# Kernel tuning notes

Hardware: AMD Instinct MI355X
Metric: run time of the kernel (lower is better)

## Reference

```python
import jax, jax.numpy as jnp
import numpy as np

N_NODES = 50000
N_EDGES = 800000
IN_DIM = 100

def setup_inputs() -> dict:
    key = jax.random.key(0)
    ks = jax.random.split(key, 12)
    nf = jax.random.normal(ks[0], (3, IN_DIM), dtype=jnp.float32)
    tid = jax.random.randint(ks[1], (N_NODES,), 0, 4)
    xr = jax.random.normal(ks[2], (N_NODES, IN_DIM), dtype=jnp.float32)
    # nodes of type 0/1/2 get exact prototype rows; type 3 ('edge') gets random rows
    x = jnp.where((tid < 3)[:, None], nf[jnp.clip(tid, 0, 2)], xr)
    edge_index = jax.random.randint(ks[3], (2, N_EDGES), 0, N_NODES, dtype=jnp.int32)
    def w(k, fi, fo):
        return jax.random.normal(k, (fi, fo), dtype=jnp.float32) * (1.0 / np.sqrt(fi))
    return {
        'x': x, 'node_feature': nf, 'edge_index': edge_index,
        'W1': w(ks[4], 100, 512), 'b1': jnp.zeros((512,), jnp.float32),
        'W2': w(ks[5], 512, 256), 'b2': jnp.zeros((256,), jnp.float32),
        'W3': w(ks[6], 256, 128), 'b3': jnp.zeros((128,), jnp.float32),
        'W4': w(ks[7], 128, 200), 'b4': jnp.zeros((200,), jnp.float32),
    }

def _gcn_forward(x, edge_index, W1, b1, W2, b2, W3, b3, W4, b4):
    N = x.shape[0]
    loop = jnp.arange(N, dtype=edge_index.dtype)
    src = jnp.concatenate([edge_index[0], loop])
    dst = jnp.concatenate([edge_index[1], loop])
    deg = jax.ops.segment_sum(jnp.ones_like(src, dtype=x.dtype), dst, num_segments=N)
    dinv = jnp.where(deg > 0, jax.lax.rsqrt(deg), 0.0)
    norm = dinv[src] * dinv[dst]  # symmetric GCN normalization with self-loops
    def gcn(h, W, b):
        h = h @ W
        agg = jax.ops.segment_sum(h[src] * norm[:, None], dst, num_segments=N)
        return agg + b
    out = jax.nn.relu(gcn(x, W1, b1))
    out = jax.nn.relu(gcn(out, W2, b2))
    out = jax.nn.relu(gcn(out, W3, b3))
    out = jax.nn.relu(gcn(out, W4, b4))
    return out

def _cat_mean(x, out, node_feature):
    # Vectorized replacement of the per-node python loop: output slot order is
    # init(nf0)->0, accept(nf2)->1, edge(other)->2, common(nf1)->3, matching the
    # original append order when all groups are nonempty.
    eq = jnp.all(x[:, None, :] == node_feature[None, :, :], axis=-1)  # [N,3]
    group = jnp.where(eq[:, 0], 0, jnp.where(eq[:, 1], 3, jnp.where(eq[:, 2], 1, 2)))
    sums = jax.ops.segment_sum(out, group, num_segments=4)            # [4,D]
    cnt = jax.ops.segment_sum(jnp.ones((x.shape[0],), out.dtype), group, num_segments=4)
    means = jnp.where(cnt[:, None] > 0, sums / jnp.maximum(cnt, 1.0)[:, None], 0.0)
    return means.reshape(1, -1)  # [1, 4*D]

def reference(x, node_feature, edge_index, W1, b1, W2, b2, W3, b3, W4, b4):
    out = _gcn_forward(x, edge_index, W1, b1, W2, b2, W3, b3, W4, b4)
    return _cat_mean(x, out, node_feature)
```

## Files before the change

kernel.cpp:

```cpp
#include <hip/hip_runtime.h>
#include <stdint.h>

typedef __attribute__((ext_vector_type(8))) short bf16x8;
typedef __attribute__((ext_vector_type(4))) float f32x4;

__device__ __forceinline__ float bf2f(ushort h) {
    union { uint u; float f; } v; v.u = ((uint)h) << 16; return v.f;
}
__device__ __forceinline__ ushort f2bf(float f) {
    union { float f; uint u; } v; v.f = f;
    uint u = v.u;
    return (ushort)((u + 0x7fffu + ((u >> 16) & 1u)) >> 16);
}

__device__ __forceinline__ void gll(const ushort* g, ushort* l) {
    __builtin_amdgcn_global_load_lds(
        (const __attribute__((address_space(1))) void*)g,
        (__attribute__((address_space(3))) void*)l, 16, 0, 0);
}

template <int VEC>
__device__ __forceinline__ void ldbf(const ushort* p, float* v) {
    if constexpr (VEC == 4) {
        uint2 u = *(const uint2*)p;
        v[0] = bf2f((ushort)(u.x & 0xffffu));
        v[1] = bf2f((ushort)(u.x >> 16));
        v[2] = bf2f((ushort)(u.y & 0xffffu));
        v[3] = bf2f((ushort)(u.y >> 16));
    } else {
        uint4 u = *(const uint4*)p;
        v[0] = bf2f((ushort)(u.x & 0xffffu));
        v[1] = bf2f((ushort)(u.x >> 16));
        v[2] = bf2f((ushort)(u.y & 0xffffu));
        v[3] = bf2f((ushort)(u.y >> 16));
        v[4] = bf2f((ushort)(u.z & 0xffffu));
        v[5] = bf2f((ushort)(u.z >> 16));
        v[6] = bf2f((ushort)(u.w & 0xffffu));
        v[7] = bf2f((ushort)(u.w >> 16));
    }
}


__device__ __forceinline__ void tr2_one(const float* __restrict__ W,
                                        ushort* __restrict__ WTh, ushort* __restrict__ WTl,
                                        int K, int Nc, int KP, int idx) {
    int n = idx / KP, k = idx % KP;
    float w = (n < Nc && k < K) ? W[(size_t)k * Nc + n] : 0.0f;
    ushort hi = f2bf(w);
    ushort lo = f2bf(w - bf2f(hi));
    WTh[idx] = hi;
    WTl[idx] = lo;
}

__global__ void k_init(const uint* __restrict__ xu, const uint* __restrict__ nfu,
                       ushort* __restrict__ xb, int* __restrict__ gid, int NN,
                       const int* __restrict__ dst, int E, int* __restrict__ deg,
                       const float* __restrict__ W1, const float* __restrict__ W2,
                       const float* __restrict__ W3, const float* __restrict__ W4,
                       ushort* __restrict__ WT1h, ushort* __restrict__ WT1l,
                       ushort* __restrict__ WT2h, ushort* __restrict__ WT2l,
                       ushort* __restrict__ WT3h, ushort* __restrict__ WT3l,
                       ushort* __restrict__ WT4h, ushort* __restrict__ WT4l,
                       int PB, int EB) {
    int b = blockIdx.x;
    if (b < PB) {
        int wid = b * 4 + (threadIdx.x >> 6);
        int lane = threadIdx.x & 63;
        if (wid >= NN) return;
        int c0 = lane * 2;
        uint w = 0u;
        int m0 = 1, m1 = 1, m2 = 1;
        if (c0 < 100) {
            uint2 xv = *(const uint2*)&xu[(size_t)wid * 100 + c0];
            uint2 a = *(const uint2*)&nfu[c0];
            uint2 bb = *(const uint2*)&nfu[100 + c0];
            uint2 c = *(const uint2*)&nfu[200 + c0];
            m0 = (xv.x == a.x) & (xv.y == a.y);
            m1 = (xv.x == bb.x) & (xv.y == bb.y);
            m2 = (xv.x == c.x) & (xv.y == c.y);
            w = (uint)f2bf(__uint_as_float(xv.x)) | ((uint)f2bf(__uint_as_float(xv.y)) << 16);
        }
        int e0 = __all(m0), e1 = __all(m1), e2 = __all(m2);
        *(uint*)&xb[(size_t)wid * 128 + c0] = w;
        if (lane == 0) gid[wid] = e0 ? 0 : (e1 ? 3 : (e2 ? 1 : 2));
    } else if (b < PB + EB) {
        int e = (b - PB) * 256 + threadIdx.x;
        if (e < E) atomicAdd(&deg[dst[e]], 1);
    } else {
        int idx = (b - PB - EB) * 256 + threadIdx.x;
        if (idx < 65536) tr2_one(W1, WT1h, WT1l, 100, 512, 128, idx);
        else if (idx < 196608) tr2_one(W2, WT2h, WT2l, 512, 256, 512, idx - 65536);
        else if (idx < 229376) tr2_one(W3, WT3h, WT3l, 256, 128, 256, idx - 196608);
        else if (idx < 262144) tr2_one(W4, WT4h, WT4l, 128, 200, 128, idx - 229376);
    }
}


__global__ void k_scanA(const int* __restrict__ deg, int* __restrict__ offs,
                        int* __restrict__ bsum, float* __restrict__ dinv,
                        const int* __restrict__ gid, int* __restrict__ gcnt, int NN) {
    __shared__ int lds[256];
    __shared__ int cnt4[4];
    int t = threadIdx.x;
    if (t < 4) cnt4[t] = 0;
    int i = blockIdx.x * 256 + t;
    int v = (i < NN) ? deg[i] : 0;
    if (i < NN) dinv[i] = 1.0f / sqrtf((float)(v + 1));
    lds[t] = v;
    __syncthreads();
    if (i < NN) atomicAdd(&cnt4[gid[i]], 1);
    for (int d = 1; d < 256; d <<= 1) {
        int u = (t >= d) ? lds[t - d] : 0;
        __syncthreads();
        lds[t] += u;
        __syncthreads();
    }
    if (i < NN) offs[i] = lds[t] - v;
    if (t == 255) bsum[blockIdx.x] = lds[255];
    __syncthreads();
    if (t < 4 && cnt4[t]) atomicAdd(&gcnt[t], cnt4[t]);
}


__global__ void k_fill(const int* __restrict__ src, const int* __restrict__ dst, int E,
                       const float* __restrict__ dinv, const int* __restrict__ offs,
                       const int* __restrict__ bsum,
                       int* __restrict__ cur, uint2* __restrict__ epk, int NN, int NB,
                       int* __restrict__ goffs) {
    __shared__ int sex[256];
    int t = threadIdx.x;
    int v = (t < NB) ? bsum[t] : 0;
    sex[t] = v;
    __syncthreads();
    for (int d = 1; d < 256; d <<= 1) {
        int u = (t >= d) ? sex[t - d] : 0;
        __syncthreads();
        sex[t] += u;
        __syncthreads();
    }
    int incl = sex[t];
    __syncthreads();
    sex[t] = incl - v;
    __syncthreads();
    int i = blockIdx.x * 256 + t;
    if (i < NN) goffs[i] = offs[i] + sex[i >> 8];
    if (i >= E) return;
    int s = src[i], d = dst[i];
    int p = offs[d] + sex[d >> 8] + atomicAdd(&cur[d], 1);
    epk[p] = make_uint2((uint)s, __float_as_uint(dinv[s] * dinv[d]));
}


template <int D, bool BR>
__global__ void k_aggs(const ushort* __restrict__ H, ushort* __restrict__ outb,
                       const float* __restrict__ dinv, const int* __restrict__ offs,
                       const int* __restrict__ deg, const uint2* __restrict__ epk,
                       const float* __restrict__ bias, int NN, int NNpad) {
    constexpr int VEC = D / 32;
    int wid = (int)((blockIdx.x * blockDim.x + threadIdx.x) >> 6);
    int lane = threadIdx.x & 63;
    int half = lane >> 5, sl = lane & 31;
    if (wid >= NNpad) return;
    int c0 = sl * VEC;
    ushort* op = outb + (size_t)wid * D + c0;
    if (wid >= NN) {
        if (half == 0) {
            if (VEC == 4) *(uint2*)op = make_uint2(0u, 0u);
            else { uint4 z; z.x = z.y = z.z = z.w = 0u; *(uint4*)op = z; }
        }
        return;
    }
    float acc[VEC];
#pragma unroll
    for (int j = 0; j < VEC; ++j) acc[j] = 0.0f;
    int beg = offs[wid], d = deg[wid];
    if (half == 0) {
        float t0[VEC];
        ldbf<VEC>(H + (size_t)wid * D + c0, t0);
        float di = dinv[wid];
        float sw = di * di;
#pragma unroll
        for (int j = 0; j < VEC; ++j) acc[j] = sw * t0[j];
    }
    int d0 = (d + 1) >> 1;
    int e = beg + half * d0;
    int end = e + (half ? (d - d0) : d0);
    for (; e + 3 < end; e += 4) {
        uint2 q0 = epk[e], q1 = epk[e + 1], q2 = epk[e + 2], q3 = epk[e + 3];
        float t0[VEC], t1[VEC], t2[VEC], t3[VEC];
        ldbf<VEC>(H + (size_t)q0.x * D + c0, t0);
        ldbf<VEC>(H + (size_t)q1.x * D + c0, t1);
        ldbf<VEC>(H + (size_t)q2.x * D + c0, t2);
        ldbf<VEC>(H + (size_t)q3.x * D + c0, t3);
        float w0 = __uint_as_float(q0.y), w1 = __uint_as_float(q1.y);
        float w2 = __uint_as_float(q2.y), w3 = __uint_as_float(q3.y);
#pragma unroll
        for (int j = 0; j < VEC; ++j) acc[j] += w0 * t0[j];
#pragma unroll
        for (int j = 0; j < VEC; ++j) acc[j] += w1 * t1[j];
#pragma unroll
        for (int j = 0; j < VEC; ++j) acc[j] += w2 * t2[j];
#pragma unroll
        for (int j = 0; j < VEC; ++j) acc[j] += w3 * t3[j];
    }
    for (; e < end; ++e) {
        uint2 q0 = epk[e];
        float t0[VEC];
        ldbf<VEC>(H + (size_t)q0.x * D + c0, t0);
        float w0 = __uint_as_float(q0.y);
#pragma unroll
        for (int j = 0; j < VEC; ++j) acc[j] += w0 * t0[j];
    }
#pragma unroll
    for (int j = 0; j < VEC; ++j) acc[j] += __shfl_xor(acc[j], 32);
    if (half == 0) {
        ushort r[VEC];
#pragma unroll
        for (int j = 0; j < VEC; ++j) {
            float v = acc[j];
            if (BR) v = fmaxf(v + bias[c0 + j], 0.0f);
            r[j] = f2bf(v);
        }
        if (VEC == 4) {
            uint2 w;
            w.x = (uint)r[0] | ((uint)r[1] << 16);
            w.y = (uint)r[2] | ((uint)r[3] << 16);
            *(uint2*)op = w;
        } else {
            uint4 w;
            w.x = (uint)r[0] | ((uint)r[1] << 16);
            w.y = (uint)r[2] | ((uint)r[3] << 16);
            w.z = (uint)r[4] | ((uint)r[5] << 16);
            w.w = (uint)r[6] | ((uint)r[7] << 16);
            *(uint4*)op = w;
        }
    }
}


template <bool BR, int OUT>
__global__ __launch_bounds__(256) void k_gemm(
        const ushort* __restrict__ A,
        const ushort* __restrict__ Bh, const ushort* __restrict__ Bl,
        const float* __restrict__ bias,
        ushort* __restrict__ Cb,
        int Nc, int K, int tNb,
        const int* __restrict__ gid, float* __restrict__ gsum, int NN) {
    __shared__ union {
        ushort st[3][128 * 32];
        float epi[64 * 132];
    } sm;
    __shared__ int gcode[64];
    int bm = blockIdx.x / tNb, bn = blockIdx.x % tNb;
    int m0 = bm * 128, n0 = bn * 128;
    int wv = threadIdx.x >> 6, lane = threadIdx.x & 63;
    int l15 = lane & 15, quad = lane >> 4;
    const ushort* gsrc;
    ushort* ldst;
    int ng;
    if (wv == 0)      { gsrc = A  + (size_t)m0 * K;        ldst = sm.st[0];        ng = 4; }
    else if (wv == 1) { gsrc = A  + (size_t)(m0 + 64) * K; ldst = sm.st[0] + 2048; ng = 4; }
    else if (wv == 2) { gsrc = Bh + (size_t)n0 * K;        ldst = sm.st[1];        ng = 8; }
    else              { gsrc = Bl + (size_t)n0 * K;        ldst = sm.st[2];        ng = 8; }
    const ushort* gBase = gsrc + (size_t)(lane >> 2) * K + (lane & 3) * 8;
    int wm = (wv >> 1) * 64, wn = (wv & 1) * 64;
    const ushort* sA_ = sm.st[0];
    const ushort* sBh_ = sm.st[1];
    const ushort* sBl_ = sm.st[2];
    f32x4 acc[4][4] = {};
    for (int k0 = 0; k0 < K; k0 += 32) {
        for (int i = 0; i < ng; ++i)
            gll(gBase + (size_t)(16 * i) * K + k0, ldst + i * 512);
        __syncthreads();
        bf16x8 Af[4], Bfh[4], Bfl[4];
#pragma unroll
        for (int i = 0; i < 4; ++i) {
            int ra = (wm + 16 * i + l15) * 32 + quad * 8;
            int rb = (wn + 16 * i + l15) * 32 + quad * 8;
            Af[i]  = *(const bf16x8*)(sA_ + ra);
            Bfh[i] = *(const bf16x8*)(sBh_ + rb);
            Bfl[i] = *(const bf16x8*)(sBl_ + rb);
        }
#pragma unroll
        for (int mi = 0; mi < 4; ++mi)
#pragma unroll
            for (int ni = 0; ni < 4; ++ni) {
                acc[mi][ni] = __builtin_amdgcn_mfma_f32_16x16x32_bf16(Af[mi], Bfh[ni], acc[mi][ni], 0, 0, 0);
                acc[mi][ni] = __builtin_amdgcn_mfma_f32_16x16x32_bf16(Af[mi], Bfl[ni], acc[mi][ni], 0, 0, 0);
            }
        __syncthreads();
    }
    float bia[4] = {0.f, 0.f, 0.f, 0.f};
    if (BR) {
#pragma unroll
        for (int ni = 0; ni < 4; ++ni) {
            int col = n0 + wn + 16 * ni + l15;
            if (col < Nc) bia[ni] = bias[col];
        }
    }
    float* epi = sm.epi;
    int t = threadIdx.x;
    float s0 = 0.f, s1 = 0.f, s2 = 0.f, s3 = 0.f;
    int colR = t & 127, rg = t >> 7;
    for (int half = 0; half < 2; ++half) {
        if ((wv >> 1) == half) {
#pragma unroll
            for (int mi = 0; mi < 4; ++mi)
#pragma unroll
                for (int r = 0; r < 4; ++r) {
                    int rl = mi * 16 + quad * 4 + r;
#pragma unroll
                    for (int ni = 0; ni < 4; ++ni) {
                        float v = acc[mi][ni][r];
                        if (BR) v = fmaxf(v + bia[ni], 0.0f);
                        epi[rl * 132 + wn + ni * 16 + l15] = v;
                    }
                }
        }
        if (OUT == 2 && t < 64) {
            int grow = m0 + half * 64 + t;
            gcode[t] = (grow < NN) ? gid[grow] : -1;
        }
        __syncthreads();
        if (OUT == 2) {
#pragma unroll 4
            for (int r = 0; r < 32; ++r) {
                int row = rg * 32 + r;
                int g = gcode[row];
                float v = epi[row * 132 + colR];
                s0 += (g == 0) ? v : 0.f;
                s1 += (g == 1) ? v : 0.f;
                s2 += (g == 2) ? v : 0.f;
                s3 += (g == 3) ? v : 0.f;
            }
        } else {
#pragma unroll
            for (int j = 0; j < 16; ++j) {
                int e = (j * 256 + t) * 2;
                int rl = e >> 7, cl = e & 127;
                int grow = m0 + half * 64 + rl;
                int gcol = n0 + cl;
                float v0 = epi[rl * 132 + cl];
                float v1 = epi[rl * 132 + cl + 1];
                *(uint*)&Cb[(size_t)grow * Nc + gcol] = (uint)f2bf(v0) | ((uint)f2bf(v1) << 16);
            }
        }
        __syncthreads();
    }
    if (OUT == 2) {
        if (rg == 1) {
            epi[colR * 4 + 0] = s0; epi[colR * 4 + 1] = s1;
            epi[colR * 4 + 2] = s2; epi[colR * 4 + 3] = s3;
        }
        __syncthreads();
        if (rg == 0) {
            s0 += epi[colR * 4 + 0]; s1 += epi[colR * 4 + 1];
            s2 += epi[colR * 4 + 2]; s3 += epi[colR * 4 + 3];
            int gcol = n0 + colR;
            if (gcol < Nc) {
                atomicAdd(&gsum[0 * Nc + gcol], s0);
                atomicAdd(&gsum[1 * Nc + gcol], s1);
                atomicAdd(&gsum[2 * Nc + gcol], s2);
                atomicAdd(&gsum[3 * Nc + gcol], s3);
            }
        }
    }
}


__global__ void k_final(const float* __restrict__ gsum, const int* __restrict__ gcnt,
                        float* __restrict__ out) {
    int j = blockIdx.x * blockDim.x + threadIdx.x;
    if (j >= 800) return;
    int c = gcnt[j / 200];
    out[j] = (c > 0) ? gsum[j] / (float)c : 0.0f;
}


extern "C" void kernel_launch(void* const* d_in, const int* in_sizes, int n_in,
                              void* d_out, int out_size, void* d_ws, size_t ws_size,
                              hipStream_t stream) {
    const float* x  = (const float*)d_in[0];
    const float* nf = (const float*)d_in[1];
    const int* ei   = (const int*)d_in[2];
    const float* W1 = (const float*)d_in[3];
    const float* b1 = (const float*)d_in[4];
    const float* W2 = (const float*)d_in[5];
    const float* b2 = (const float*)d_in[6];
    const float* W3 = (const float*)d_in[7];
    const float* b3 = (const float*)d_in[8];
    const float* W4 = (const float*)d_in[9];
    const float* b4 = (const float*)d_in[10];
    float* out = (float*)d_out;

    const int NN = in_sizes[0] / 100;
    const int E  = in_sizes[2] / 2;
    const int MPAD = ((NN + 127) / 128) * 128;
    const int NB = (NN + 255) / 256;
    const int PB = (NN + 3) / 4;
    const int EB = (E + 255) / 256;
    const int TB = 1024;
    const int* src = ei;
    const int* dst = ei + E;

    char* p = (char*)d_ws;
    auto alloc = [&](size_t bytes) -> char* {
        char* r = p;
        p += (bytes + 255) & ~(size_t)255;
        return r;
    };
    char* zz = p;
    int*   deg  = (int*)alloc((size_t)NN * 4);
    int*   cur  = (int*)alloc((size_t)NN * 4);
    float* gsum = (float*)alloc(800 * 4);
    int*   gcnt = (int*)alloc(256);
    size_t zz_bytes = (size_t)(p - zz);
    float* dinv = (float*)alloc((size_t)NN * 4);
    int*   offs = (int*)alloc((size_t)NN * 4);
    int*   goffs = (int*)alloc((size_t)NN * 4);
    int*   bsum = (int*)alloc(1024);
    int*   gid  = (int*)alloc((size_t)NN * 4);
    uint2* epk  = (uint2*)alloc((size_t)E * 8);
    ushort* WT1h = (ushort*)alloc((size_t)512 * 128 * 2);
    ushort* WT1l = (ushort*)alloc((size_t)512 * 128 * 2);
    ushort* WT2h = (ushort*)alloc((size_t)256 * 512 * 2);
    ushort* WT2l = (ushort*)alloc((size_t)256 * 512 * 2);
    ushort* WT3h = (ushort*)alloc((size_t)128 * 256 * 2);
    ushort* WT3l = (ushort*)alloc((size_t)128 * 256 * 2);
    ushort* WT4h = (ushort*)alloc((size_t)256 * 128 * 2);
    ushort* WT4l = (ushort*)alloc((size_t)256 * 128 * 2);
    ushort* xb = (ushort*)alloc((size_t)NN * 128 * 2);
    ushort* P1 = (ushort*)alloc((size_t)MPAD * 128 * 2);
    ushort* H1 = (ushort*)alloc((size_t)MPAD * 512 * 2);
    ushort* T2 = (ushort*)alloc((size_t)MPAD * 256 * 2);
    ushort* H2 = (ushort*)alloc((size_t)MPAD * 256 * 2);
    ushort* T3 = (ushort*)alloc((size_t)MPAD * 128 * 2);
    ushort* H3 = (ushort*)alloc((size_t)MPAD * 128 * 2);
    ushort* P4 = (ushort*)alloc((size_t)MPAD * 128 * 2);

    hipMemsetAsync(zz, 0, zz_bytes, stream);

    k_init<<<PB + EB + TB, 256, 0, stream>>>(
        (const uint*)x, (const uint*)nf, xb, gid, NN, dst, E, deg,
        W1, W2, W3, W4, WT1h, WT1l, WT2h, WT2l, WT3h, WT3l, WT4h, WT4l, PB, EB);
    k_scanA<<<NB, 256, 0, stream>>>(deg, offs, bsum, dinv, gid, gcnt, NN);
    k_fill<<<EB, 256, 0, stream>>>(src, dst, E, dinv, offs, bsum, cur, epk, NN, NB, goffs);

    int aggBlocks = MPAD / 4;
    int mB = MPAD / 128;

    k_aggs<128, false><<<aggBlocks, 256, 0, stream>>>(xb, P1, dinv, goffs, deg, epk, nullptr, NN, MPAD);
    k_gemm<true, 1><<<mB * 4, 256, 0, stream>>>(P1, WT1h, WT1l, b1, H1, 512, 128, 4, nullptr, nullptr, 0);
    k_gemm<false, 1><<<mB * 2, 256, 0, stream>>>(H1, WT2h, WT2l, nullptr, T2, 256, 512, 2, nullptr, nullptr, 0);
    k_aggs<256, true><<<aggBlocks, 256, 0, stream>>>(T2, H2, dinv, goffs, deg, epk, b2, NN, MPAD);
    k_gemm<false, 1><<<mB * 1, 256, 0, stream>>>(H2, WT3h, WT3l, nullptr, T3, 128, 256, 1, nullptr, nullptr, 0);
    k_aggs<128, true><<<aggBlocks, 256, 0, stream>>>(T3, H3, dinv, goffs, deg, epk, b3, NN, MPAD);
    k_aggs<128, false><<<aggBlocks, 256, 0, stream>>>(H3, P4, dinv, goffs, deg, epk, nullptr, NN, MPAD);
    k_gemm<true, 2><<<mB * 2, 256, 0, stream>>>(P4, WT4h, WT4l, b4, nullptr, 200, 128, 2, gid, gsum, NN);

    k_final<<<4, 256, 0, stream>>>(gsum, gcnt, out);
}
```

Before: 454.8 us.

## Rewrite aggregation as one wave per row with 2 columns per lane

The gather-aggregate kernel now gives each of the 64 lanes two bf16 columns of a 128-wide slice and walks all of a node's edges in one pass. The old scheme split the edges between two half-waves and combined them with a shuffle. Edge records are read with nontemporal loads and processed in unrolled chunks of 8/4/2/1. The 256-wide layer is handled as two 128-column launches over the same strided buffer. This removes the cross-half reduction and the wide vector loads, at the cost of narrower 4-byte gathers per lane and reading the edge list twice for layer 2.

```diff
diff --git a/kernel.cpp b/kernel.cpp
--- a/kernel.cpp
+++ b/kernel.cpp
@@ -17,27 +17,6 @@
     __builtin_amdgcn_global_load_lds(
         (const __attribute__((address_space(1))) void*)g,
         (__attribute__((address_space(3))) void*)l, 16, 0, 0);
-}
-
-template <int VEC>
-__device__ __forceinline__ void ldbf(const ushort* p, float* v) {
-    if constexpr (VEC == 4) {
-        uint2 u = *(const uint2*)p;
-        v[0] = bf2f((ushort)(u.x & 0xffffu));
-        v[1] = bf2f((ushort)(u.x >> 16));
-        v[2] = bf2f((ushort)(u.y & 0xffffu));
-        v[3] = bf2f((ushort)(u.y >> 16));
-    } else {
-        uint4 u = *(const uint4*)p;
-        v[0] = bf2f((ushort)(u.x & 0xffffu));
-        v[1] = bf2f((ushort)(u.x >> 16));
-        v[2] = bf2f((ushort)(u.y & 0xffffu));
-        v[3] = bf2f((ushort)(u.y >> 16));
-        v[4] = bf2f((ushort)(u.z & 0xffffu));
-        v[5] = bf2f((ushort)(u.z >> 16));
-        v[6] = bf2f((ushort)(u.w & 0xffffu));
-        v[7] = bf2f((ushort)(u.w >> 16));
-    }
 }
 
 
@@ -151,90 +130,69 @@
 }
 
 
-template <int D, bool BR>
-__global__ void k_aggs(const ushort* __restrict__ H, ushort* __restrict__ outb,
-                       const float* __restrict__ dinv, const int* __restrict__ offs,
-                       const int* __restrict__ deg, const uint2* __restrict__ epk,
-                       const float* __restrict__ bias, int NN, int NNpad) {
-    constexpr int VEC = D / 32;
+__device__ __forceinline__ uint2 ldnt_u2(const uint2* p) {
+    union { unsigned long long ll; uint2 v; } r;
+    r.ll = __builtin_nontemporal_load((const unsigned long long*)p);
+    return r.v;
+}
+
+__device__ __forceinline__ void fma2(uint u, float w, float& a0, float& a1) {
+    union { uint u; float f; } lo, hi;
+    lo.u = u << 16;
+    hi.u = u & 0xffff0000u;
+    a0 = fmaf(w, lo.f, a0);
+    a1 = fmaf(w, hi.f, a1);
+}
+
+template <int UN, int LD>
+__device__ __forceinline__ void agg_step(const ushort* __restrict__ Hc,
+                                         const uint2* __restrict__ epk, int e,
+                                         float& a0, float& a1) {
+    uint2 q[UN];
+#pragma unroll
+    for (int i = 0; i < UN; ++i) q[i] = ldnt_u2(epk + e + i);
+    uint u[UN];
+#pragma unroll
+    for (int i = 0; i < UN; ++i) u[i] = *(const uint*)(Hc + (size_t)q[i].x * LD);
+#pragma unroll
+    for (int i = 0; i < UN; ++i) fma2(u[i], __uint_as_float(q[i].y), a0, a1);
+}
+
+template <int LD, bool BR>
+__global__ __launch_bounds__(256) void k_aggs(
+        const ushort* __restrict__ H, ushort* __restrict__ outb,
+        const float* __restrict__ dinv, const int* __restrict__ offs,
+        const int* __restrict__ deg, const uint2* __restrict__ epk,
+        const float* __restrict__ bias, int NN, int NNpad) {
     int wid = (int)((blockIdx.x * blockDim.x + threadIdx.x) >> 6);
     int lane = threadIdx.x & 63;
-    int half = lane >> 5, sl = lane & 31;
     if (wid >= NNpad) return;
-    int c0 = sl * VEC;
-    ushort* op = outb + (size_t)wid * D + c0;
+    int c0 = lane * 2;
+    ushort* op = outb + (size_t)wid * LD + c0;
     if (wid >= NN) {
-        if (half == 0) {
-            if (VEC == 4) *(uint2*)op = make_uint2(0u, 0u);
-            else { uint4 z; z.x = z.y = z.z = z.w = 0u; *(uint4*)op = z; }
-        }
+        __builtin_nontemporal_store(0u, (uint*)op);
         return;
     }
-    float acc[VEC];
-#pragma unroll
-    for (int j = 0; j < VEC; ++j) acc[j] = 0.0f;
-    int beg = offs[wid], d = deg[wid];
-    if (half == 0) {
-        float t0[VEC];
-        ldbf<VEC>(H + (size_t)wid * D + c0, t0);
+    const ushort* Hc = H + c0;
+    float a0 = 0.0f, a1 = 0.0f;
+    {
         float di = dinv[wid];
         float sw = di * di;
-#pragma unroll
-        for (int j = 0; j < VEC; ++j) acc[j] = sw * t0[j];
-    }
-    int d0 = (d + 1) >> 1;
-    int e = beg + half * d0;
-    int end = e + (half ? (d - d0) : d0);
-    for (; e + 3 < end; e += 4) {
-        uint2 q0 = epk[e], q1 = epk[e + 1], q2 = epk[e + 2], q3 = epk[e + 3];
-        float t0[VEC], t1[VEC], t2[VEC], t3[VEC];
-        ldbf<VEC>(H + (size_t)q0.x * D + c0, t0);
-        ldbf<VEC>(H + (size_t)q1.x * D + c0, t1);
-        ldbf<VEC>(H + (size_t)q2.x * D + c0, t2);
-        ldbf<VEC>(H + (size_t)q3.x * D + c0, t3);
-        float w0 = __uint_as_float(q0.y), w1 = __uint_as_float(q1.y);
-        float w2 = __uint_as_float(q2.y), w3 = __uint_as_float(q3.y);
-#pragma unroll
-        for (int j = 0; j < VEC; ++j) acc[j] += w0 * t0[j];
-#pragma unroll
-        for (int j = 0; j < VEC; ++j) acc[j] += w1 * t1[j];
-#pragma unroll
-        for (int j = 0; j < VEC; ++j) acc[j] += w2 * t2[j];
-#pragma unroll
-        for (int j = 0; j < VEC; ++j) acc[j] += w3 * t3[j];
-    }
-    for (; e < end; ++e) {
-        uint2 q0 = epk[e];
-        float t0[VEC];
-        ldbf<VEC>(H + (size_t)q0.x * D + c0, t0);
-        float w0 = __uint_as_float(q0.y);
-#pragma unroll
-        for (int j = 0; j < VEC; ++j) acc[j] += w0 * t0[j];
-    }
-#pragma unroll
-    for (int j = 0; j < VEC; ++j) acc[j] += __shfl_xor(acc[j], 32);
-    if (half == 0) {
-        ushort r[VEC];
-#pragma unroll
-        for (int j = 0; j < VEC; ++j) {
-            float v = acc[j];
-            if (BR) v = fmaxf(v + bias[c0 + j], 0.0f);
-            r[j] = f2bf(v);
-        }
-        if (VEC == 4) {
-            uint2 w;
-            w.x = (uint)r[0] | ((uint)r[1] << 16);
-            w.y = (uint)r[2] | ((uint)r[3] << 16);
-            *(uint2*)op = w;
-        } else {
-            uint4 w;
-            w.x = (uint)r[0] | ((uint)r[1] << 16);
-            w.y = (uint)r[2] | ((uint)r[3] << 16);
-            w.z = (uint)r[4] | ((uint)r[5] << 16);
-            w.w = (uint)r[6] | ((uint)r[7] << 16);
-            *(uint4*)op = w;
-        }
-    }
+        uint u = *(const uint*)(Hc + (size_t)wid * LD);
+        fma2(u, sw, a0, a1);
+    }
+    int e = offs[wid];
+    int end = e + deg[wid];
+    for (; e + 8 <= end; e += 8) agg_step<8, LD>(Hc, epk, e, a0, a1);
+    if (e + 4 <= end) { agg_step<4, LD>(Hc, epk, e, a0, a1); e += 4; }
+    if (e + 2 <= end) { agg_step<2, LD>(Hc, epk, e, a0, a1); e += 2; }
+    if (e < end) agg_step<1, LD>(Hc, epk, e, a0, a1);
+    if (BR) {
+        a0 = fmaxf(a0 + bias[c0], 0.0f);
+        a1 = fmaxf(a1 + bias[c0 + 1], 0.0f);
+    }
+    uint w = (uint)f2bf(a0) | ((uint)f2bf(a1) << 16);
+    __builtin_nontemporal_store(w, (uint*)op);
 }
 
 
@@ -453,6 +411,7 @@
     k_gemm<true, 1><<<mB * 4, 256, 0, stream>>>(P1, WT1h, WT1l, b1, H1, 512, 128, 4, nullptr, nullptr, 0);
     k_gemm<false, 1><<<mB * 2, 256, 0, stream>>>(H1, WT2h, WT2l, nullptr, T2, 256, 512, 2, nullptr, nullptr, 0);
     k_aggs<256, true><<<aggBlocks, 256, 0, stream>>>(T2, H2, dinv, goffs, deg, epk, b2, NN, MPAD);
+    k_aggs<256, true><<<aggBlocks, 256, 0, stream>>>(T2 + 128, H2 + 128, dinv, goffs, deg, epk, b2 + 128, NN, MPAD);
     k_gemm<false, 1><<<mB * 1, 256, 0, stream>>>(H2, WT3h, WT3l, nullptr, T3, 128, 256, 1, nullptr, nullptr, 0);
     k_aggs<128, true><<<aggBlocks, 256, 0, stream>>>(T3, H3, dinv, goffs, deg, epk, b3, NN, MPAD);
     k_aggs<128, false><<<aggBlocks, 256, 0, stream>>>(H3, P4, dinv, goffs, deg, epk, nullptr, NN, MPAD);
```

Measured after the change: 462.8 us. About the same (+1.7%).
